# Performance work log

Measured on AMD Instinct MI355X. Metric: run time of the kernel, lower is better.

Reference implementation:

```python
import jax, jax.numpy as jnp
import numpy as np

# MPO config: input_size = output_size = 4096 = 16**3, num_cores = 3, rank = 16
D_IN = 16    # in_leg_dim
D_OUT = 16   # out_leg_dim
RANK = 16
IN_SIZE = D_IN ** 3
OUT_SIZE = D_OUT ** 3
B = 2048     # flattened batch*seq tokens


def setup_inputs() -> dict:
    key = jax.random.key(0)
    ks = jax.random.split(key, 5)
    bound = 1.0 / np.sqrt(IN_SIZE)
    u = lambda k, shp: jax.random.uniform(k, shp, jnp.float32, -bound, bound)
    return {
        "x": jax.random.normal(ks[0], (B, IN_SIZE), dtype=jnp.float32),
        "first_core": u(ks[1], (D_IN, RANK, D_OUT)),        # (in, rank_right, out)
        "middle_core": u(ks[2], (D_IN, RANK, RANK, D_OUT)),  # (in, rank_left, rank_right, out)
        "last_core": u(ks[3], (D_IN, RANK, D_OUT)),          # (in, rank_left, out)
        "bias": u(ks[4], (OUT_SIZE,)),
    }


def reference(x, first_core, middle_core, last_core, bias):
    # Faithful MPO chain contraction, same edge wiring and order as the
    # tensornetwork-based original (contract input legs left-to-right,
    # threading the bond/rank index through the cores).
    xr = x.reshape(-1, D_IN, D_IN, D_IN)                       # (b, i, j, k)
    # contract input leg i with first core -> legs (b, j, k, r, m)
    t = jnp.einsum('bijk,irm->bjkrm', xr, first_core)
    # contract input leg j and bond r with middle core -> (b, k, m, s, n)
    t = jnp.einsum('bjkrm,jrsn->bkmsn', t, middle_core)
    # contract input leg k and bond s with last core -> (b, m, n, o)
    t = jnp.einsum('bkmsn,kso->bmno', t, last_core)
    return t.reshape(-1, OUT_SIZE) + bias
```

## Files before the change

### kernel.cpp

```cpp
#include <hip/hip_runtime.h>

#define DLEG 16
#define IN_SIZE 4096
#define OUT_SIZE 4096
#define BATCH 2048

#define SX 25.4f
#define SW 1.1545455e6f

typedef __attribute__((ext_vector_type(4))) int i32x4;

__device__ __forceinline__ signed char f2i8(float f, float s) {
  int q = __float2int_rn(f * s);
  q = q > 127 ? 127 : (q < -127 ? -127 : q);
  return (signed char)q;
}

__device__ __forceinline__ void async_copy16(const void* g, void* l) {
  __builtin_amdgcn_global_load_lds(
      (const __attribute__((address_space(1))) void*)g,
      (__attribute__((address_space(3))) void*)l, 16, 0, 0);
}

__global__ __launch_bounds__(256) void k_prep(
    const float* __restrict__ x, const float* __restrict__ fc,
    const float* __restrict__ mc, const float* __restrict__ lc,
    signed char* __restrict__ xi, signed char* __restrict__ wt) {
  __shared__ float fc_s[256];
  __shared__ float mc_s[4096];
  __shared__ float a_s[1024];
  const int t = threadIdx.x;

  if (blockIdx.x < 2048) {
    const int idx = blockIdx.x * 256 + t;
    const int l = idx & 63;
    const int kt = (idx >> 6) & 63;
    const int m16 = idx >> 12;
    const int row = m16 * 16 + (l & 15);
    const int kb = kt * 64 + (l >> 4) * 16;
    const float4* xp = (const float4*)(x + (size_t)row * 4096 + kb);
    union { int4 v; signed char c[16]; } u;
#pragma unroll
    for (int q = 0; q < 4; ++q) {
      const float4 f = xp[q];
      u.c[q * 4 + 0] = f2i8(f.x, SX);
      u.c[q * 4 + 1] = f2i8(f.y, SX);
      u.c[q * 4 + 2] = f2i8(f.z, SX);
      u.c[q * 4 + 3] = f2i8(f.w, SX);
    }
    ((int4*)xi)[idx] = u.v;
    return;
  }

  const int idx = blockIdx.x - 2048;
  const int b = idx & 255;
  const int mg = idx >> 8;
  const int i = b >> 4, j = b & 15;

  fc_s[t] = fc[i * 256 + t];
#pragma unroll
  for (int q = 0; q < 16; ++q) mc_s[q * 256 + t] = mc[j * 4096 + q * 256 + t];
  __syncthreads();

  {
    const int n = t >> 4, s = t & 15;
    float accm[4] = {0.f, 0.f, 0.f, 0.f};
#pragma unroll
    for (int r = 0; r < 16; ++r) {
      const float mcv = mc_s[r * 256 + s * 16 + n];
#pragma unroll
      for (int ml = 0; ml < 4; ++ml)
        accm[ml] = fmaf(fc_s[r * 16 + mg * 4 + ml], mcv, accm[ml]);
    }
#pragma unroll
    for (int ml = 0; ml < 4; ++ml) a_s[ml * 256 + n * 16 + s] = accm[ml];
  }
  __syncthreads();

  const int k = t & 15, op = (t >> 4) & 3, sel = t >> 6;
  float lcr[4][16];
#pragma unroll
  for (int oo = 0; oo < 4; ++oo)
#pragma unroll
    for (int s = 0; s < 16; ++s)
      lcr[oo][s] = lc[k * 256 + s * 16 + op * 4 + oo];

#pragma unroll
  for (int ml = 0; ml < 4; ++ml) {
#pragma unroll
    for (int nn = 0; nn < 4; ++nn) {
      const int n = sel * 4 + nn;
      const float4* ap2 = (const float4*)&a_s[ml * 256 + n * 16];
      float av[16];
      ((float4*)av)[0] = ap2[0];
      ((float4*)av)[1] = ap2[1];
      ((float4*)av)[2] = ap2[2];
      ((float4*)av)[3] = ap2[3];
      float accv[4] = {0.f, 0.f, 0.f, 0.f};
#pragma unroll
      for (int s = 0; s < 16; ++s) {
#pragma unroll
        for (int oo = 0; oo < 4; ++oo)
          accv[oo] = fmaf(av[s], lcr[oo][s], accv[oo]);
      }
      const size_t colbase =
          (size_t)((mg * 4 + ml) * 256 + n * 16 + op * 4);
#pragma unroll
      for (int oo = 0; oo < 4; ++oo)
        wt[(colbase + oo) * 4096 + b * 16 + k] = f2i8(accv[oo], SW);
    }
  }
}


#define ALOAD(SET)                                                            \
  { _Pragma("unroll") for (int mi = 0; mi < 4; ++mi) {                        \
      SET[mi * 2]     = *(const i32x4*)(ap[mi]);                              \
      SET[mi * 2 + 1] = *(const i32x4*)(ap[mi] + 1024);                       \
      ap[mi] += 2048;                                                         \
  } }

#define BREAD                                                                 \
  { _Pragma("unroll") for (int ni = 0; ni < 4; ++ni)                          \
      bf[ni] = *(const i32x4*)&Br[(brow + ni * 16) * 128 + s0f];              \
    _Pragma("unroll") for (int ni = 0; ni < 4; ++ni)                          \
      bf[4 + ni] = *(const i32x4*)&Br[(brow + ni * 16) * 128 + s1f]; }

#define STAGE_B4(KT)                                                          \
  { _Pragma("unroll") for (int u = 0; u < 4; ++u)                             \
      async_copy16(wg[u] + (KT), Bw + woff[u]); }

#define MFMA32(CA)                                                            \
  __builtin_amdgcn_s_setprio(1);                                              \
  _Pragma("unroll") for (int ks = 0; ks < 2; ++ks)                            \
    _Pragma("unroll") for (int mi = 0; mi < 4; ++mi)                          \
      _Pragma("unroll") for (int ni = 0; ni < 4; ++ni)                        \
        acc[mi][ni] = __builtin_amdgcn_mfma_i32_16x16x64_i8(                  \
            CA[mi * 2 + ks], bf[ks * 4 + ni], acc[mi][ni], 0, 0, 0);          \
  __builtin_amdgcn_s_setprio(0)

#define ROT3                                                                  \
  { signed char* tb = Br; Br = Bn; Bn = Bw; Bw = tb; }

#define TILE(CURA, NXTA, VN, DOSTAGE, DOLOAD)                                 \
  if (DOSTAGE) { STAGE_B4(ktS); }                                             \
  if (DOLOAD)  { ALOAD(NXTA); }                                               \
  asm volatile("s_waitcnt lgkmcnt(0)" ::: "memory");                          \
  asm volatile("s_waitcnt vmcnt(" #VN ")" ::: "memory");                      \
  __builtin_amdgcn_s_barrier();                                               \
  __builtin_amdgcn_sched_barrier(0);                                          \
  BREAD;                                                                      \
  MFMA32(CURA)

__global__ __launch_bounds__(512, 2) void k_gemm(
    const signed char* __restrict__ X,
    const signed char* __restrict__ Wt,
    const float* __restrict__ bias,
    float* __restrict__ out) {
  __shared__ __align__(16) signed char Bs[3][256 * 128];

  const int t = threadIdx.x;
  const int l = t & 63, w = t >> 6;
  const int wm = w >> 2, wn = w & 3;
  const int m0 = blockIdx.y * 128, n0 = blockIdx.x * 256;

  const signed char* wg[4];
  int woff[4];
#pragma unroll
  for (int u = 0; u < 4; ++u) {
    const int c = u * 512 + t;
    const int row = c >> 3;
    const int slot = (c & 7) ^ (row & 7);
    wg[u] = Wt + (size_t)(n0 + row) * 4096 + slot * 16;
    woff[u] = c * 16;
  }

  const signed char* ap[4];
#pragma unroll
  for (int mi = 0; mi < 4; ++mi)
    ap[mi] = X + (size_t)(blockIdx.y * 8 + wm * 4 + mi) * 65536 + l * 16;

  const int brow = wn * 64 + (l & 15);
  const int lk = l >> 4;
  const int lx = l & 7;
  const int s0f = (lk ^ lx) * 16;
  const int s1f = ((4 + lk) ^ lx) * 16;

  i32x4 acc[4][4];
#pragma unroll
  for (int a = 0; a < 4; ++a)
#pragma unroll
    for (int c = 0; c < 4; ++c) acc[a][c] = (i32x4){0, 0, 0, 0};

  i32x4 Pa[8], Qa[8], bf[8];

  signed char *Br = Bs[0], *Bn = Bs[1], *Bw = Bs[2];

  {
    signed char* sv = Bw;
    Bw = Bs[0];
    STAGE_B4(0);
    Bw = Bs[1];
    STAGE_B4(128);
    Bw = sv;
  }
  ALOAD(Pa);

  int ktS = 256;
#pragma unroll 1
  for (int tt = 0; tt < 15; ++tt) {
    TILE(Pa, Qa, 12, 1, 1);
    ROT3; ktS += 128;
    TILE(Qa, Pa, 12, 1, 1);
    ROT3; ktS += 128;
  }
  TILE(Pa, Qa, 8, 0, 1);
  ROT3;
  asm volatile("s_waitcnt lgkmcnt(0)" ::: "memory");
  asm volatile("s_waitcnt vmcnt(0)" ::: "memory");
  __builtin_amdgcn_s_barrier();
  __builtin_amdgcn_sched_barrier(0);
  BREAD;
  MFMA32(Qa);

  const float inv = 1.0f / (SX * SW);
#pragma unroll
  for (int ni = 0; ni < 4; ++ni) {
    const int col = n0 + wn * 64 + ni * 16 + (l & 15);
    const float bv = bias[col];
#pragma unroll
    for (int mi = 0; mi < 4; ++mi) {
      const int row = m0 + wm * 64 + mi * 16 + (l >> 4) * 4;
#pragma unroll
      for (int r = 0; r < 4; ++r)
        out[(size_t)(row + r) * 4096 + col] =
            (float)acc[mi][ni][r] * inv + bv;
    }
  }
}

extern "C" void kernel_launch(void* const* d_in, const int* in_sizes, int n_in,
                              void* d_out, int out_size, void* d_ws,
                              size_t ws_size, hipStream_t stream) {
  const float* x    = (const float*)d_in[0];
  const float* fc   = (const float*)d_in[1];
  const float* mc   = (const float*)d_in[2];
  const float* lc   = (const float*)d_in[3];
  const float* bias = (const float*)d_in[4];
  float* out = (float*)d_out;

  signed char* xi = (signed char*)d_ws;
  signed char* wt = xi + (size_t)BATCH * IN_SIZE;

  k_prep<<<2048 + 1024, 256, 0, stream>>>(x, fc, mc, lc, xi, wt);
  k_gemm<<<dim3(OUT_SIZE / 256, BATCH / 128), 512, 0, stream>>>(xi, wt, bias,
                                                                out);
}
```

Measured before the change: 145.5 us.

## Swap GEMM operand roles: stage activations in LDS, stream weights to registers

The int8 GEMM now keeps the activation tile (128 rows) in a triple-buffered LDS ring and streams pre-swizzled weight fragments directly from global memory into registers. Prep writes activations row-major and writes weights in the fragment-friendly layout. The GEMM moves to 128x128 tiles with 256 threads, a 1D grid with block-index swizzling for L2 locality, and reorders waits so LDS staging overlaps MFMA. This changes the LDS footprint, occupancy and the pipeline's wait structure, and risks uncovered latency on the direct global loads.

```diff
diff --git a/kernel.cpp b/kernel.cpp
--- a/kernel.cpp
+++ b/kernel.cpp
@@ -33,12 +33,7 @@
 
   if (blockIdx.x < 2048) {
     const int idx = blockIdx.x * 256 + t;
-    const int l = idx & 63;
-    const int kt = (idx >> 6) & 63;
-    const int m16 = idx >> 12;
-    const int row = m16 * 16 + (l & 15);
-    const int kb = kt * 64 + (l >> 4) * 16;
-    const float4* xp = (const float4*)(x + (size_t)row * 4096 + kb);
+    const float4* xp = (const float4*)x + (size_t)idx * 4;
     union { int4 v; signed char c[16]; } u;
 #pragma unroll
     for (int q = 0; q < 4; ++q) {
@@ -85,6 +80,7 @@
     for (int s = 0; s < 16; ++s)
       lcr[oo][s] = lc[k * 256 + s * 16 + op * 4 + oo];
 
+  const int ktw = b >> 2, lhi = (b & 3) * 16;
 #pragma unroll
   for (int ml = 0; ml < 4; ++ml) {
 #pragma unroll
@@ -103,84 +99,91 @@
         for (int oo = 0; oo < 4; ++oo)
           accv[oo] = fmaf(av[s], lcr[oo][s], accv[oo]);
       }
-      const size_t colbase =
-          (size_t)((mg * 4 + ml) * 256 + n * 16 + op * 4);
-#pragma unroll
-      for (int oo = 0; oo < 4; ++oo)
-        wt[(colbase + oo) * 4096 + b * 16 + k] = f2i8(accv[oo], SW);
-    }
-  }
-}
-
-
-#define ALOAD(SET)                                                            \
+      const int n16 = (mg * 4 + ml) * 16 + n;
+#pragma unroll
+      for (int oo = 0; oo < 4; ++oo) {
+        const size_t F =
+            ((size_t)((n16 * 64 + ktw) * 64) + lhi + op * 4 + oo) * 16 + k;
+        wt[F] = f2i8(accv[oo], SW);
+      }
+    }
+  }
+}
+
+
+#define BLOAD(SET)                                                            \
+  { _Pragma("unroll") for (int ni = 0; ni < 4; ++ni) {                        \
+      SET[ni * 2]     = *(const i32x4*)(bp[ni]);                              \
+      SET[ni * 2 + 1] = *(const i32x4*)(bp[ni] + 1024);                       \
+      bp[ni] += 2048;                                                         \
+  } }
+
+#define AREAD                                                                 \
   { _Pragma("unroll") for (int mi = 0; mi < 4; ++mi) {                        \
-      SET[mi * 2]     = *(const i32x4*)(ap[mi]);                              \
-      SET[mi * 2 + 1] = *(const i32x4*)(ap[mi] + 1024);                       \
-      ap[mi] += 2048;                                                         \
+      af[mi * 2]     = *(const i32x4*)&Ac[(arow + mi * 16) * 128 + s0f];      \
+      af[mi * 2 + 1] = *(const i32x4*)&Ac[(arow + mi * 16) * 128 + s1f];      \
   } }
 
-#define BREAD                                                                 \
-  { _Pragma("unroll") for (int ni = 0; ni < 4; ++ni)                          \
-      bf[ni] = *(const i32x4*)&Br[(brow + ni * 16) * 128 + s0f];              \
-    _Pragma("unroll") for (int ni = 0; ni < 4; ++ni)                          \
-      bf[4 + ni] = *(const i32x4*)&Br[(brow + ni * 16) * 128 + s1f]; }
-
-#define STAGE_B4(KT)                                                          \
+#define STAGE_A(BUF, KT)                                                      \
   { _Pragma("unroll") for (int u = 0; u < 4; ++u)                             \
-      async_copy16(wg[u] + (KT), Bw + woff[u]); }
-
-#define MFMA32(CA)                                                            \
+      async_copy16(xg[u] + (KT), (BUF) + xoff[u]); }
+
+#define MFMA32(CB)                                                            \
   __builtin_amdgcn_s_setprio(1);                                              \
   _Pragma("unroll") for (int ks = 0; ks < 2; ++ks)                            \
     _Pragma("unroll") for (int mi = 0; mi < 4; ++mi)                          \
       _Pragma("unroll") for (int ni = 0; ni < 4; ++ni)                        \
         acc[mi][ni] = __builtin_amdgcn_mfma_i32_16x16x64_i8(                  \
-            CA[mi * 2 + ks], bf[ks * 4 + ni], acc[mi][ni], 0, 0, 0);          \
+            af[mi * 2 + ks], CB[ni * 2 + ks], acc[mi][ni], 0, 0, 0);          \
   __builtin_amdgcn_s_setprio(0)
 
 #define ROT3                                                                  \
-  { signed char* tb = Br; Br = Bn; Bn = Bw; Bw = tb; }
-
-#define TILE(CURA, NXTA, VN, DOSTAGE, DOLOAD)                                 \
-  if (DOSTAGE) { STAGE_B4(ktS); }                                             \
-  if (DOLOAD)  { ALOAD(NXTA); }                                               \
-  asm volatile("s_waitcnt lgkmcnt(0)" ::: "memory");                          \
+  { signed char* ta = Ac; Ac = An; An = Aw; Aw = ta; }
+
+#define TILE(CURB, NXTB, VN, DOB, DOS)                                        \
   asm volatile("s_waitcnt vmcnt(" #VN ")" ::: "memory");                      \
   __builtin_amdgcn_s_barrier();                                               \
   __builtin_amdgcn_sched_barrier(0);                                          \
-  BREAD;                                                                      \
-  MFMA32(CURA)
-
-__global__ __launch_bounds__(512, 2) void k_gemm(
+  if (DOB) { BLOAD(NXTB); }                                                   \
+  if (DOS) { STAGE_A(Aw, ktS); }                                              \
+  AREAD;                                                                      \
+  __builtin_amdgcn_sched_barrier(0);                                          \
+  MFMA32(CURB)
+
+__global__ __launch_bounds__(256, 2) void k_gemm(
     const signed char* __restrict__ X,
     const signed char* __restrict__ Wt,
     const float* __restrict__ bias,
     float* __restrict__ out) {
-  __shared__ __align__(16) signed char Bs[3][256 * 128];
+  __shared__ __align__(16) signed char As[3][128 * 128];
 
   const int t = threadIdx.x;
   const int l = t & 63, w = t >> 6;
-  const int wm = w >> 2, wn = w & 3;
-  const int m0 = blockIdx.y * 128, n0 = blockIdx.x * 256;
-
-  const signed char* wg[4];
-  int woff[4];
+  const int wm = w >> 1, wn = w & 1;
+
+  const int bid = blockIdx.x;
+  const int swz = (bid & 7) * 64 + (bid >> 3);
+  const int bn = swz >> 4;
+  const int bm = swz & 15;
+  const int m0 = bm * 128;
+
+  const signed char* xg[4];
+  int xoff[4];
 #pragma unroll
   for (int u = 0; u < 4; ++u) {
-    const int c = u * 512 + t;
+    const int c = u * 256 + t;
     const int row = c >> 3;
     const int slot = (c & 7) ^ (row & 7);
-    wg[u] = Wt + (size_t)(n0 + row) * 4096 + slot * 16;
-    woff[u] = c * 16;
-  }
-
-  const signed char* ap[4];
-#pragma unroll
-  for (int mi = 0; mi < 4; ++mi)
-    ap[mi] = X + (size_t)(blockIdx.y * 8 + wm * 4 + mi) * 65536 + l * 16;
-
-  const int brow = wn * 64 + (l & 15);
+    xg[u] = X + (size_t)(m0 + row) * 4096 + slot * 16;
+    xoff[u] = c * 16;
+  }
+
+  const signed char* bp[4];
+#pragma unroll
+  for (int ni = 0; ni < 4; ++ni)
+    bp[ni] = Wt + (size_t)(bn * 8 + wn * 4 + ni) * 65536 + l * 16;
+
+  const int arow = wm * 64 + (l & 15);
   const int lk = l >> 4;
   const int lx = l & 7;
   const int s0f = (lk ^ lx) * 16;
@@ -192,38 +195,28 @@
 #pragma unroll
     for (int c = 0; c < 4; ++c) acc[a][c] = (i32x4){0, 0, 0, 0};
 
-  i32x4 Pa[8], Qa[8], bf[8];
-
-  signed char *Br = Bs[0], *Bn = Bs[1], *Bw = Bs[2];
-
-  {
-    signed char* sv = Bw;
-    Bw = Bs[0];
-    STAGE_B4(0);
-    Bw = Bs[1];
-    STAGE_B4(128);
-    Bw = sv;
-  }
-  ALOAD(Pa);
-
+  i32x4 Pb[8], Qb[8], af[8];
+
+  BLOAD(Pb);
+  STAGE_A(As[0], 0);
+  STAGE_A(As[1], 128);
+
+  signed char *Ac = As[0], *An = As[1], *Aw = As[2];
   int ktS = 256;
+
 #pragma unroll 1
   for (int tt = 0; tt < 15; ++tt) {
-    TILE(Pa, Qa, 12, 1, 1);
+    TILE(Pb, Qb, 4, 1, 1);
     ROT3; ktS += 128;
-    TILE(Qa, Pa, 12, 1, 1);
+    TILE(Qb, Pb, 4, 1, 1);
     ROT3; ktS += 128;
   }
-  TILE(Pa, Qa, 8, 0, 1);
+  TILE(Pb, Qb, 4, 1, 0);
   ROT3;
-  asm volatile("s_waitcnt lgkmcnt(0)" ::: "memory");
-  asm volatile("s_waitcnt vmcnt(0)" ::: "memory");
-  __builtin_amdgcn_s_barrier();
-  __builtin_amdgcn_sched_barrier(0);
-  BREAD;
-  MFMA32(Qa);
+  TILE(Qb, Pb, 0, 0, 0);
 
   const float inv = 1.0f / (SX * SW);
+  const int n0 = bn * 128;
 #pragma unroll
   for (int ni = 0; ni < 4; ++ni) {
     const int col = n0 + wn * 64 + ni * 16 + (l & 15);
@@ -253,6 +246,5 @@
   signed char* wt = xi + (size_t)BATCH * IN_SIZE;
 
   k_prep<<<2048 + 1024, 256, 0, stream>>>(x, fc, mc, lc, xi, wt);
-  k_gemm<<<dim3(OUT_SIZE / 256, BATCH / 128), 512, 0, stream>>>(xi, wt, bias,
-                                                                out);
-}
+  k_gemm<<<512, 256, 0, stream>>>(xi, wt, bias, out);
+}
```

Result: faster. 140.5 us (-3.4%).
